# Kernel optimization log

Measured on AMD Instinct MI355X. Metric: run time of the kernel, lower is better.

Reference implementation:

```python
import jax, jax.numpy as jnp
import numpy as np

B, D, H, C = 8192, 384, 256, 6
K_MIN, K_MAX = 4, 16
LN_EPS = 1e-5


def setup_inputs() -> dict:
    key = jax.random.key(0)
    ks = jax.random.split(key, 6)
    s = lambda k, shape: (jax.random.normal(k, shape, jnp.float32) * 0.05)
    return {
        "x": jax.random.normal(ks[0], (B, D), jnp.float32),
        "W_proj": s(ks[1], (D, H)), "b_proj": jnp.zeros((H,), jnp.float32),
        "W_tau": s(ks[2], (D, 1)), "b_tau": jnp.zeros((1,), jnp.float32),
        "W_res": s(ks[3], (H, H)), "b_res": jnp.zeros((H,), jnp.float32),
        "ln_g": jnp.ones((H,), jnp.float32), "ln_b": jnp.zeros((H,), jnp.float32),
        "W_fc": s(ks[4], (H, C)), "b_fc": jnp.zeros((C,), jnp.float32),
    }


def reference(x, W_proj, b_proj, W_tau, b_tau, W_res, b_res, ln_g, ln_b, W_fc, b_fc):
    # adaptive k per sample (torch path casts to int -> non-differentiable)
    tau = jax.nn.sigmoid(x @ W_tau + b_tau)[:, 0]                      # [B]
    k = jax.lax.stop_gradient(
        jnp.clip(jnp.round(K_MAX - (K_MAX - K_MIN) * tau), 1, K_MAX)
    ).astype(jnp.int32)                                                # [B]

    # pairwise squared distances (same nearest-neighbor ordering as cdist)
    sq = jnp.sum(x * x, axis=-1)                                       # [B]
    d2 = sq[:, None] + sq[None, :] - 2.0 * (x @ x.T)                   # [B,B]
    _, idx = jax.lax.top_k(-jax.lax.stop_gradient(d2), K_MAX)          # [B,K_MAX] nearest (incl. self)

    h = jax.nn.relu(x @ W_proj + b_proj)                               # [B,H]

    # ragged top-k mean via fixed K_MAX gather + position mask
    gathered = h[idx]                                                  # [B,K_MAX,H]
    mask = (jnp.arange(K_MAX)[None, :] < k[:, None]).astype(h.dtype)   # [B,K_MAX]
    agg = jnp.einsum('bkh,bk->bh', gathered, mask) / k[:, None].astype(h.dtype)

    r = jax.nn.relu(agg @ W_res + b_res)                               # [B,H]
    z = h + r
    mu = jnp.mean(z, axis=-1, keepdims=True)
    var = jnp.var(z, axis=-1, keepdims=True)
    zn = (z - mu) / jnp.sqrt(var + LN_EPS)
    return (zn * ln_g + ln_b) @ W_fc + b_fc                            # [B,C]
```

## Files before the change

kernel.cpp:

```cpp
#include <hip/hip_runtime.h>
#include <hip/hip_fp16.h>
#include <math.h>

#define NROWS 8192
#define DDIM 384
#define HDIM 256
#define CDIM 6
#define LN_EPS 1e-5f
#define DSTR 138
#define NTILES ((NROWS/128) * (NROWS/128 + 1) / 2)
#define NGEMM1 ((NROWS/128) * (HDIM/128))

typedef short bf16x8 __attribute__((ext_vector_type(8)));
typedef float f32x4 __attribute__((ext_vector_type(4)));
typedef unsigned short u16x8 __attribute__((ext_vector_type(8)));
typedef unsigned short u16x4 __attribute__((ext_vector_type(4)));
typedef unsigned short u16x2 __attribute__((ext_vector_type(2)));

__device__ __forceinline__ bool dj_better(float d1, int j1, float d2, int j2) {
    return (d1 < d2) || (d1 == d2 && j1 < j2);
}

__device__ __forceinline__ unsigned int umin_(unsigned int a, unsigned int b) { return a < b ? a : b; }
__device__ __forceinline__ unsigned int umax_(unsigned int a, unsigned int b) { return a > b ? a : b; }

__device__ __forceinline__ unsigned short map16f(float v) {
    union { _Float16 f; unsigned short u; } c;
    c.f = (_Float16)v;
    unsigned short b = c.u;
    return (unsigned short)(b ^ (unsigned short)((((short)b) >> 15) | 0x8000));
}

__device__ __forceinline__ float unmap16(unsigned int m16b) {
    unsigned short fb = (m16b & 0x8000u) ? (unsigned short)(m16b ^ 0x8000u)
                                         : (unsigned short)(~m16b);
    union { unsigned short u; _Float16 f; } cv; cv.u = fb;
    return (float)cv.f;
}

__device__ __forceinline__ unsigned short rne_bf16(float v) {
    unsigned int u = __float_as_uint(v);
    u += 0x7fffu + ((u >> 16) & 1u);
    return (unsigned short)(u >> 16);
}

__device__ __forceinline__ void ins8(
    unsigned int& s0, unsigned int& s1, unsigned int& s2, unsigned int& s3,
    unsigned int& s4, unsigned int& s5, unsigned int& s6, unsigned int& s7,
    unsigned int& m, unsigned int key)
{
    if (key < m) {
        s0 = (s0 == m) ? key : s0;
        s1 = (s1 == m) ? key : s1;
        s2 = (s2 == m) ? key : s2;
        s3 = (s3 == m) ? key : s3;
        s4 = (s4 == m) ? key : s4;
        s5 = (s5 == m) ? key : s5;
        s6 = (s6 == m) ? key : s6;
        s7 = (s7 == m) ? key : s7;
        m = umax_(umax_(umax_(s0, s1), umax_(s2, s3)),
                  umax_(umax_(s4, s5), umax_(s6, s7)));
    }
}

__device__ __forceinline__ unsigned int max8_(
    unsigned int s0, unsigned int s1, unsigned int s2, unsigned int s3,
    unsigned int s4, unsigned int s5, unsigned int s6, unsigned int s7)
{
    return umax_(umax_(umax_(s0, s1), umax_(s2, s3)),
                 umax_(umax_(s4, s5), umax_(s6, s7)));
}

__device__ __forceinline__ void sins8(
    unsigned int& s0, unsigned int& s1, unsigned int& s2, unsigned int& s3,
    unsigned int& s4, unsigned int& s5, unsigned int& s6, unsigned int& s7,
    unsigned int key)
{
    unsigned int t = umin_(s0, key);
    s0 = umax_(t, s1); t = umin_(t, s1);
    s1 = umax_(t, s2); t = umin_(t, s2);
    s2 = umax_(t, s3); t = umin_(t, s3);
    s3 = umax_(t, s4); t = umin_(t, s4);
    s4 = umax_(t, s5); t = umin_(t, s5);
    s5 = umax_(t, s6); t = umin_(t, s6);
    s6 = umax_(t, s7); s7 = umin_(t, s7);
}

#define CE_(a, b) { unsigned int hi_ = umax_(a, b), lo_ = umin_(a, b); a = hi_; b = lo_; }
#define SORT8_DESC(s0, s1, s2, s3, s4, s5, s6, s7) \
    CE_(s0, s1) CE_(s2, s3) CE_(s4, s5) CE_(s6, s7) \
    CE_(s0, s2) CE_(s1, s3) CE_(s4, s6) CE_(s5, s7) \
    CE_(s1, s2) CE_(s5, s6) CE_(s0, s4) CE_(s3, s7) \
    CE_(s1, s5) CE_(s2, s6) \
    CE_(s1, s4) CE_(s3, s6) \
    CE_(s2, s4) CE_(s3, s5) \
    CE_(s3, s4)

__global__ void __launch_bounds__(256) prep_kernel(
    const float* __restrict__ x, const float* __restrict__ W_tau,
    const float* __restrict__ b_tau, unsigned short* __restrict__ xb,
    float* __restrict__ sq, int* __restrict__ kk,
    const float* __restrict__ Wp, unsigned short* __restrict__ wpT,
    const float* __restrict__ Wr, unsigned short* __restrict__ wrT)
{
    int tid = threadIdx.x;
    if (blockIdx.x < NROWS / 4) {
        int wave = tid >> 6, lane = tid & 63;
        int row = blockIdx.x * 4 + wave;
        const float* xr = x + (size_t)row * DDIM;
        unsigned short* xbr = xb + (size_t)row * DDIM;
        float s = 0.f, tp = 0.f;
        #pragma unroll
        for (int q = 0; q < 6; ++q) {
            float v = xr[lane + 64 * q];
            xbr[lane + 64 * q] = rne_bf16(v);
            s = fmaf(v, v, s);
            tp = fmaf(v, W_tau[lane + 64 * q], tp);
        }
        #pragma unroll
        for (int off = 32; off > 0; off >>= 1) {
            s += __shfl_xor(s, off);
            tp += __shfl_xor(tp, off);
        }
        if (lane == 0) {
            sq[row] = s;
            float u = tp + b_tau[0];
            float tau = 1.f / (1.f + expf(-u));
            float kf = rintf(16.f - 12.f * tau);
            int k = (int)kf;
            k = min(16, max(1, k));
            kk[row] = k;
        }
    } else {
        int i = (blockIdx.x - NROWS / 4) * 256 + tid;
        if (i < DDIM * HDIM) {
            int k = i / HDIM, n = i % HDIM;
            wpT[(size_t)n * DDIM + k] = rne_bf16(Wp[i]);
        } else {
            int j = i - DDIM * HDIM;
            if (j < HDIM * HDIM) {
                int k = j / HDIM, n = j % HDIM;
                wrT[(size_t)n * HDIM + k] = rne_bf16(Wr[j]);
            }
        }
    }
}

__device__ __forceinline__ void gemm_kloop(
    const unsigned short* __restrict__ A, const unsigned short* __restrict__ B,
    const int K, const int rowbase, const int nbase,
    unsigned short* S, f32x4 (&acc)[4][4])
{
    const int tid = threadIdx.x;
    const int wave = tid >> 6;
    const int lane = tid & 63;
    const int wr = (wave >> 1) * 64;
    const int wc = (wave & 1) * 64;
    const int m16 = lane & 15;
    const int kq = lane >> 4;
    const int er0 = tid >> 2;
    const int er1 = 64 + (tid >> 2);
    const int eko = tid & 3;
    const int NK = K >> 5;

    auto stage = [&](int kb, int set) {
        const int k0 = kb * 32;
        char* Ad = (char*)S + set * 8192;
        char* Bd = (char*)S + 16384 + set * 8192;
        __builtin_amdgcn_global_load_lds(
            (const __attribute__((address_space(1))) void*)(A + (size_t)(rowbase + er0) * K + k0 + eko * 8),
            (__attribute__((address_space(3))) void*)(Ad + (wave * 64) * 16), 16, 0, 0);
        __builtin_amdgcn_global_load_lds(
            (const __attribute__((address_space(1))) void*)(A + (size_t)(rowbase + er1) * K + k0 + eko * 8),
            (__attribute__((address_space(3))) void*)(Ad + (256 + wave * 64) * 16), 16, 0, 0);
        __builtin_amdgcn_global_load_lds(
            (const __attribute__((address_space(1))) void*)(B + (size_t)(nbase + er0) * K + k0 + eko * 8),
            (__attribute__((address_space(3))) void*)(Bd + (wave * 64) * 16), 16, 0, 0);
        __builtin_amdgcn_global_load_lds(
            (const __attribute__((address_space(1))) void*)(B + (size_t)(nbase + er1) * K + k0 + eko * 8),
            (__attribute__((address_space(3))) void*)(Bd + (256 + wave * 64) * 16), 16, 0, 0);
    };

    stage(0, 0);
    stage(1, 1);
    asm volatile("s_waitcnt vmcnt(4)" ::: "memory");
    __builtin_amdgcn_s_barrier();
    __builtin_amdgcn_sched_barrier(0);

    for (int kb = 0; kb < NK; ++kb) {
        const int cur = kb & 1;
        const unsigned short* Ab = S + cur * 4096;
        const unsigned short* Bb = S + 8192 + cur * 4096;
        bf16x8 af[4], bfr[4];
        #pragma unroll
        for (int s = 0; s < 4; ++s) {
            af[s]  = *(const bf16x8*)&Ab[(wr + s * 16 + m16) * 32 + kq * 8];
            bfr[s] = *(const bf16x8*)&Bb[(wc + s * 16 + m16) * 32 + kq * 8];
        }
        #pragma unroll
        for (int si = 0; si < 4; ++si)
            #pragma unroll
            for (int sj = 0; sj < 4; ++sj)
                acc[si][sj] = __builtin_amdgcn_mfma_f32_16x16x32_bf16(
                    af[si], bfr[sj], acc[si][sj], 0, 0, 0);
        asm volatile("s_waitcnt lgkmcnt(0)" ::: "memory");
        __builtin_amdgcn_s_barrier();
        __builtin_amdgcn_sched_barrier(0);
        if (kb + 2 < NK) {
            stage(kb + 2, cur);
            asm volatile("s_waitcnt vmcnt(4)" ::: "memory");
            __builtin_amdgcn_s_barrier();
            __builtin_amdgcn_sched_barrier(0);
        } else if (kb + 1 < NK) {
            asm volatile("s_waitcnt vmcnt(0)" ::: "memory");
            __builtin_amdgcn_s_barrier();
            __builtin_amdgcn_sched_barrier(0);
        }
    }
}

__device__ __forceinline__ void gemm_epilogue(
    const float* __restrict__ bias, float* __restrict__ out,
    unsigned short* __restrict__ hb, const int rowbase, const int nbase,
    f32x4 (&acc)[4][4])
{
    const int lane = threadIdx.x & 63;
    const int wave = threadIdx.x >> 6;
    const int wr = (wave >> 1) * 64;
    const int wc = (wave & 1) * 64;
    const int m16 = lane & 15;
    const int kq = lane >> 4;
    #pragma unroll
    for (int sj = 0; sj < 4; ++sj) {
        int c = nbase + wc + sj * 16 + m16;
        float bc = bias[c];
        #pragma unroll
        for (int si = 0; si < 4; ++si) {
            int r = rowbase + wr + si * 16 + kq * 4;
            #pragma unroll
            for (int v = 0; v < 4; ++v) {
                float val = fmaxf(acc[si][sj][v] + bc, 0.f);
                out[(size_t)(r + v) * HDIM + c] = val;
                if (hb) hb[(size_t)(r + v) * HDIM + c] = rne_bf16(val);
            }
        }
    }
}

__global__ void __launch_bounds__(256) mfma_gemm_bias_relu_kernel(
    const unsigned short* __restrict__ A, const unsigned short* __restrict__ WT,
    const float* __restrict__ bias, float* __restrict__ out,
    unsigned short* __restrict__ hb, int K)
{
    __shared__ __align__(16) unsigned short S[16384];
    f32x4 acc[4][4];
    #pragma unroll
    for (int a = 0; a < 4; ++a)
        #pragma unroll
        for (int b = 0; b < 4; ++b)
            acc[a][b] = (f32x4){0.f, 0.f, 0.f, 0.f};
    gemm_kloop(A, WT, K, blockIdx.x * 128, blockIdx.y * 128, S, acc);
    gemm_epilogue(bias, out, hb, blockIdx.x * 128, blockIdx.y * 128, acc);
}

__global__ void __launch_bounds__(256) dist_gemm_fused_kernel(
    const unsigned short* __restrict__ xb, const float* __restrict__ sq,
    unsigned int* __restrict__ keys,
    const unsigned short* __restrict__ wpT, const float* __restrict__ b_proj,
    float* __restrict__ h, unsigned short* __restrict__ hb)
{
    __shared__ __align__(16) unsigned short SMEM[128 * DSTR];

    f32x4 acc[4][4];
    #pragma unroll
    for (int a = 0; a < 4; ++a)
        #pragma unroll
        for (int b = 0; b < 4; ++b)
            acc[a][b] = (f32x4){0.f, 0.f, 0.f, 0.f};

    if (blockIdx.x < NGEMM1) {
        const int rb = (blockIdx.x >> 1) * 128;
        const int nb = (blockIdx.x & 1) * 128;
        gemm_kloop(xb, wpT, DDIM, rb, nb, SMEM, acc);
        gemm_epilogue(b_proj, h, hb, rb, nb, acc);
        return;
    }

    int t0 = blockIdx.x - NGEMM1;
    int t = (t0 & 7) * (NTILES / 8) + (t0 >> 3);
    int bi = (int)((sqrtf(8.f * (float)t + 1.f) - 1.f) * 0.5f);
    while ((bi + 1) * (bi + 2) / 2 <= t) ++bi;
    while (bi * (bi + 1) / 2 > t) --bi;
    int bj = t - bi * (bi + 1) / 2;

    const int tid = threadIdx.x;
    const int wave = tid >> 6;
    const int lane = tid & 63;
    const int rowbase = bi * 128;
    const int colbase = bj * 128;
    const int wr = (wave >> 1) * 64;
    const int wc = (wave & 1) * 64;
    const int m16 = lane & 15;
    const int kq = lane >> 4;

    gemm_kloop(xb, xb, DDIM, rowbase, colbase, SMEM, acc);
    __syncthreads();
    unsigned short* Dt = SMEM;

    const int sr = tid >> 1;
    const int seg = tid & 1;

    {
        float sqc[4];
        #pragma unroll
        for (int sj = 0; sj < 4; ++sj) sqc[sj] = sq[colbase + wc + sj * 16 + m16];
        #pragma unroll
        for (int si = 0; si < 4; ++si)
            #pragma unroll
            for (int sj = 0; sj < 4; ++sj) {
                int r = wr + si * 16 + kq * 4;
                int c = wc + sj * 16 + m16;
                #pragma unroll
                for (int v = 0; v < 4; ++v)
                    Dt[(r + v) * DSTR + c] = map16f(sqc[sj] - 2.0f * acc[si][sj][v]);
            }
        __syncthreads();

        const unsigned short* rowp = &Dt[sr * DSTR + seg * 64];
        const int cb0 = colbase + seg * 64;
        u16x8 c0 = *(const u16x8*)rowp;
        unsigned int s0 = ((unsigned int)c0[0] << 13) | (unsigned int)(cb0 + 0);
        unsigned int s1 = ((unsigned int)c0[1] << 13) | (unsigned int)(cb0 + 1);
        unsigned int s2 = ((unsigned int)c0[2] << 13) | (unsigned int)(cb0 + 2);
        unsigned int s3 = ((unsigned int)c0[3] << 13) | (unsigned int)(cb0 + 3);
        unsigned int s4 = ((unsigned int)c0[4] << 13) | (unsigned int)(cb0 + 4);
        unsigned int s5 = ((unsigned int)c0[5] << 13) | (unsigned int)(cb0 + 5);
        unsigned int s6 = ((unsigned int)c0[6] << 13) | (unsigned int)(cb0 + 6);
        unsigned int s7 = ((unsigned int)c0[7] << 13) | (unsigned int)(cb0 + 7);
        SORT8_DESC(s0, s1, s2, s3, s4, s5, s6, s7);
        #pragma unroll
        for (int i = 1; i < 8; ++i) {
            u16x8 ch = *(const u16x8*)(rowp + i * 8);
            int cb = cb0 + i * 8;
            #pragma unroll
            for (int e = 0; e < 8; ++e)
                sins8(s0, s1, s2, s3, s4, s5, s6, s7,
                      ((unsigned int)ch[e] << 13) | (unsigned int)(cb + e));
        }
        size_t kb = (size_t)(rowbase + sr) * 1024 + (size_t)bj * 16 + seg * 8;
        uint4 o0; o0.x = s0; o0.y = s1; o0.z = s2; o0.w = s3;
        uint4 o1; o1.x = s4; o1.y = s5; o1.z = s6; o1.w = s7;
        *(uint4*)&keys[kb] = o0;
        *(uint4*)&keys[kb + 4] = o1;
    }

    if (bi != bj) {
        __syncthreads();
        #pragma unroll
        for (int si = 0; si < 4; ++si) {
            float4 sqr4 = *(const float4*)&sq[rowbase + wr + si * 16 + kq * 4];
            float srw[4] = {sqr4.x, sqr4.y, sqr4.z, sqr4.w};
            #pragma unroll
            for (int sj = 0; sj < 4; ++sj) {
                int r = wr + si * 16 + kq * 4;
                int c = wc + sj * 16 + m16;
                unsigned short h4[4];
                #pragma unroll
                for (int v = 0; v < 4; ++v)
                    h4[v] = map16f(srw[v] - 2.0f * acc[si][sj][v]);
                *(unsigned long long*)&Dt[c * DSTR + r] = *(unsigned long long*)h4;
            }
        }
        __syncthreads();

        const unsigned short* rowp = &Dt[sr * DSTR + seg * 64];
        const int cb0 = rowbase + seg * 64;
        u16x8 c0 = *(const u16x8*)rowp;
        unsigned int s0 = ((unsigned int)c0[0] << 13) | (unsigned int)(cb0 + 0);
        unsigned int s1 = ((unsigned int)c0[1] << 13) | (unsigned int)(cb0 + 1);
        unsigned int s2 = ((unsigned int)c0[2] << 13) | (unsigned int)(cb0 + 2);
        unsigned int s3 = ((unsigned int)c0[3] << 13) | (unsigned int)(cb0 + 3);
        unsigned int s4 = ((unsigned int)c0[4] << 13) | (unsigned int)(cb0 + 4);
        unsigned int s5 = ((unsigned int)c0[5] << 13) | (unsigned int)(cb0 + 5);
        unsigned int s6 = ((unsigned int)c0[6] << 13) | (unsigned int)(cb0 + 6);
        unsigned int s7 = ((unsigned int)c0[7] << 13) | (unsigned int)(cb0 + 7);
        SORT8_DESC(s0, s1, s2, s3, s4, s5, s6, s7);
        #pragma unroll
        for (int i = 1; i < 8; ++i) {
            u16x8 ch = *(const u16x8*)(rowp + i * 8);
            int cb = cb0 + i * 8;
            #pragma unroll
            for (int e = 0; e < 8; ++e)
                sins8(s0, s1, s2, s3, s4, s5, s6, s7,
                      ((unsigned int)ch[e] << 13) | (unsigned int)(cb + e));
        }
        size_t kb = (size_t)(colbase + sr) * 1024 + (size_t)bi * 16 + seg * 8;
        uint4 o0; o0.x = s0; o0.y = s1; o0.z = s2; o0.w = s3;
        uint4 o1; o1.x = s4; o1.y = s5; o1.z = s6; o1.w = s7;
        *(uint4*)&keys[kb] = o0;
        *(uint4*)&keys[kb + 4] = o1;
    }
}

__global__ void __launch_bounds__(256) topk_rescore_agg_kernel(
    const unsigned int* __restrict__ keys, const float* __restrict__ x,
    const float* __restrict__ sq, const int* __restrict__ kk,
    const unsigned short* __restrict__ hb, unsigned short* __restrict__ aggb)
{
    const int w = threadIdx.x >> 6;
    const int row = blockIdx.x * 4 + w;
    const int lane = threadIdx.x & 63;
    __shared__ int sidx[4][16];

    const uint4* kp = (const uint4*)(keys + (size_t)row * 1024 + lane * 16);
    uint4 v0 = kp[0], v1 = kp[1];
    unsigned int s0 = v0.x, s1 = v0.y, s2 = v0.z, s3 = v0.w;
    unsigned int s4 = v1.x, s5 = v1.y, s6 = v1.z, s7 = v1.w;
    unsigned int m = max8_(s0, s1, s2, s3, s4, s5, s6, s7);
    #pragma unroll
    for (int q = 2; q < 4; ++q) {
        uint4 v = kp[q];
        unsigned int gmin = umin_(umin_(v.x, v.y), umin_(v.z, v.w));
        if (gmin < m) {
            ins8(s0, s1, s2, s3, s4, s5, s6, s7, m, v.x);
            ins8(s0, s1, s2, s3, s4, s5, s6, s7, m, v.y);
            ins8(s0, s1, s2, s3, s4, s5, s6, s7, m, v.z);
            ins8(s0, s1, s2, s3, s4, s5, s6, s7, m, v.w);
        }
    }
    unsigned int lmin = umin_(umin_(umin_(s0, s1), umin_(s2, s3)),
                              umin_(umin_(s4, s5), umin_(s6, s7)));
    unsigned int myout = 0;
    for (int t = 0; t < 32; ++t) {
        unsigned int wv = lmin;
        #pragma unroll
        for (int off = 32; off > 0; off >>= 1)
            wv = umin_(wv, (unsigned int)__shfl_xor((int)wv, off));
        if (lane == t) myout = wv;
        if (lmin == wv) {
            s0 = (s0 == wv) ? 0xFFFFFFFFu : s0;
            s1 = (s1 == wv) ? 0xFFFFFFFFu : s1;
            s2 = (s2 == wv) ? 0xFFFFFFFFu : s2;
            s3 = (s3 == wv) ? 0xFFFFFFFFu : s3;
            s4 = (s4 == wv) ? 0xFFFFFFFFu : s4;
            s5 = (s5 == wv) ? 0xFFFFFFFFu : s5;
            s6 = (s6 == wv) ? 0xFFFFFFFFu : s6;
            s7 = (s7 == wv) ? 0xFFFFFFFFu : s7;
            lmin = umin_(umin_(umin_(s0, s1), umin_(s2, s3)),
                         umin_(umin_(s4, s5), umin_(s6, s7)));
        }
    }
    int myj = (int)(myout & 8191u);
    float dscr = (lane < 32) ? unmap16(myout >> 13) : INFINITY;

    const float EPS2 = 2.5f;
    const int k = kk[row];
    float d_k   = __shfl(dscr, k);
    float d_km1 = __shfl(dscr, k - 1);
    bool cin = false, amb = false;
    if (lane < 32) {
        if (lane < k) { cin = (dscr + EPS2 <= d_k); amb = !cin; }
        else          { amb = (dscr < d_km1 + EPS2); }
    }
    unsigned long long cinmask = __ballot(cin);
    unsigned long long ambmask = __ballot(amb);
    int n_in = __popcll(cinmask);
    int msel = k - n_in;

    float d_ex = 0.f;
    if (msel > 0) {
        float xr[6];
        #pragma unroll
        for (int q = 0; q < 6; ++q) xr[q] = x[(size_t)row * DDIM + lane + 64 * q];
        float sqrow = sq[row];
        unsigned long long mm = ambmask;
        while (mm) {
            int c = (int)(__ffsll(mm) - 1);
            mm &= mm - 1;
            int j = __shfl(myj, c);
            const float* xc = x + (size_t)j * DDIM;
            float p = 0.f;
            #pragma unroll
            for (int q = 0; q < 6; ++q) p = fmaf(xr[q], xc[lane + 64 * q], p);
            #pragma unroll
            for (int off = 32; off > 0; off >>= 1) p += __shfl_xor(p, off);
            float d = sqrow + sq[j] - 2.f * p;
            if (lane == c) d_ex = d;
        }
        int selrank = 0;
        unsigned long long mm2 = ambmask;
        while (mm2) {
            int u = (int)(__ffsll(mm2) - 1);
            mm2 &= mm2 - 1;
            float du = __shfl(d_ex, u);
            int ju = __shfl(myj, u);
            if (u != lane && dj_better(du, ju, d_ex, myj)) ++selrank;
        }
        if (amb && selrank < msel)
            sidx[w][n_in + selrank] = myj;
    }
    if (cin) {
        int pos = __popcll(cinmask & ((1ull << lane) - 1ull));
        sidx[w][pos] = myj;
    }
    __syncthreads();

    float a0 = 0.f, a1 = 0.f, a2 = 0.f, a3 = 0.f;
    for (int t = 0; t < k; ++t) {
        uint2 v = *(const uint2*)(hb + (size_t)sidx[w][t] * HDIM + lane * 4);
        a0 += __uint_as_float(v.x << 16);
        a1 += __uint_as_float(v.x & 0xFFFF0000u);
        a2 += __uint_as_float(v.y << 16);
        a3 += __uint_as_float(v.y & 0xFFFF0000u);
    }
    float inv = 1.f / (float)k;
    unsigned int b0 = rne_bf16(a0 * inv);
    unsigned int b1 = rne_bf16(a1 * inv);
    unsigned int b2 = rne_bf16(a2 * inv);
    unsigned int b3 = rne_bf16(a3 * inv);
    uint2 o; o.x = b0 | (b1 << 16); o.y = b2 | (b3 << 16);
    *(uint2*)(aggb + (size_t)row * HDIM + lane * 4) = o;
}

__global__ void __launch_bounds__(256) ln_fc_kernel(
    const float* __restrict__ h, const float* __restrict__ r,
    const float* __restrict__ g, const float* __restrict__ bb,
    const float* __restrict__ W_fc, const float* __restrict__ b_fc,
    float* __restrict__ out)
{
    const int row = blockIdx.x * 4 + (threadIdx.x >> 6);
    const int lane = threadIdx.x & 63;
    const float* hp = h + (size_t)row * HDIM;
    const float* rp = r + (size_t)row * HDIM;

    float z[4];
    #pragma unroll
    for (int q = 0; q < 4; ++q)
        z[q] = hp[lane + 64 * q] + rp[lane + 64 * q];

    float s = z[0] + z[1] + z[2] + z[3];
    float s2 = z[0]*z[0] + z[1]*z[1] + z[2]*z[2] + z[3]*z[3];
    #pragma unroll
    for (int off = 32; off > 0; off >>= 1) {
        s += __shfl_xor(s, off);
        s2 += __shfl_xor(s2, off);
    }
    float mu = s / 256.f;
    float rstd = rsqrtf(s2 / 256.f - mu * mu + LN_EPS);

    float p[6] = {0.f, 0.f, 0.f, 0.f, 0.f, 0.f};
    #pragma unroll
    for (int q = 0; q < 4; ++q) {
        int i = lane + 64 * q;
        float val = (z[q] - mu) * rstd * g[i] + bb[i];
        #pragma unroll
        for (int c = 0; c < 6; ++c)
            p[c] = fmaf(val, W_fc[i * 6 + c], p[c]);
    }
    #pragma unroll
    for (int c = 0; c < 6; ++c)
        #pragma unroll
        for (int off = 32; off > 0; off >>= 1) p[c] += __shfl_xor(p[c], off);

    if (lane < 6) {
        float o = p[0];
        o = (lane == 1) ? p[1] : o;
        o = (lane == 2) ? p[2] : o;
        o = (lane == 3) ? p[3] : o;
        o = (lane == 4) ? p[4] : o;
        o = (lane == 5) ? p[5] : o;
        out[(size_t)row * CDIM + lane] = o + b_fc[lane];
    }
}

extern "C" void kernel_launch(void* const* d_in, const int* in_sizes, int n_in,
                              void* d_out, int out_size, void* d_ws, size_t ws_size,
                              hipStream_t stream) {
    const float* x      = (const float*)d_in[0];
    const float* W_proj = (const float*)d_in[1];
    const float* b_proj = (const float*)d_in[2];
    const float* W_tau  = (const float*)d_in[3];
    const float* b_tau  = (const float*)d_in[4];
    const float* W_res  = (const float*)d_in[5];
    const float* b_res  = (const float*)d_in[6];
    const float* ln_g   = (const float*)d_in[7];
    const float* ln_b   = (const float*)d_in[8];
    const float* W_fc   = (const float*)d_in[9];
    const float* b_fc   = (const float*)d_in[10];
    float* out = (float*)d_out;

    char* ws = (char*)d_ws;
    float* sq   = (float*)ws;                        ws += (size_t)NROWS * 4;
    int*   kk   = (int*)ws;                          ws += (size_t)NROWS * 4;
    float* h    = (float*)ws;                        ws += (size_t)NROWS * HDIM * 4;
    float* r    = (float*)ws;                        ws += (size_t)NROWS * HDIM * 4;
    unsigned short* xb   = (unsigned short*)ws;      ws += (size_t)NROWS * DDIM * 2;
    unsigned short* hbuf = (unsigned short*)ws;      ws += (size_t)NROWS * HDIM * 2;
    unsigned short* aggb = (unsigned short*)ws;      ws += (size_t)NROWS * HDIM * 2;
    unsigned short* wpT  = (unsigned short*)ws;      ws += (size_t)DDIM * HDIM * 2;
    unsigned short* wrT  = (unsigned short*)ws;      ws += (size_t)HDIM * HDIM * 2;
    ws = (char*)(((size_t)ws + 255) & ~(size_t)255);
    unsigned int* keys = (unsigned int*)ws;          ws += (size_t)NROWS * 1024 * 4;

    const int prepW = (DDIM * HDIM + HDIM * HDIM + 255) / 256;
    prep_kernel<<<NROWS / 4 + prepW, 256, 0, stream>>>(
        x, W_tau, b_tau, xb, sq, kk, W_proj, wpT, W_res, wrT);
    dist_gemm_fused_kernel<<<NGEMM1 + NTILES, 256, 0, stream>>>(
        xb, sq, keys, wpT, b_proj, h, hbuf);
    topk_rescore_agg_kernel<<<NROWS / 4, 256, 0, stream>>>(keys, x, sq, kk, hbuf, aggb);
    mfma_gemm_bias_relu_kernel<<<dim3(NROWS / 128, HDIM / 128), 256, 0, stream>>>(
        aggb, wrT, b_res, r, (unsigned short*)nullptr, HDIM);
    ln_fc_kernel<<<NROWS / 4, 256, 0, stream>>>(h, r, ln_g, ln_b, W_fc, b_fc, out);
}
```

Before: 223.6 us.

## Split top-k scan into dual chains and transpose per-tile key layout

```diff
diff --git a/kernel.cpp b/kernel.cpp
--- a/kernel.cpp
+++ b/kernel.cpp
@@ -10,12 +10,12 @@
 #define DSTR 138
 #define NTILES ((NROWS/128) * (NROWS/128 + 1) / 2)
 #define NGEMM1 ((NROWS/128) * (HDIM/128))
+#define KSTRIDE ((size_t)NROWS * 16)
 
 typedef short bf16x8 __attribute__((ext_vector_type(8)));
 typedef float f32x4 __attribute__((ext_vector_type(4)));
 typedef unsigned short u16x8 __attribute__((ext_vector_type(8)));
-typedef unsigned short u16x4 __attribute__((ext_vector_type(4)));
-typedef unsigned short u16x2 __attribute__((ext_vector_type(2)));
+typedef unsigned int u32x4 __attribute__((ext_vector_type(4)));
 
 __device__ __forceinline__ bool dj_better(float d1, int j1, float d2, int j2) {
     return (d1 < d2) || (d1 == d2 && j1 < j2);
@@ -71,30 +71,67 @@
                  umax_(umax_(s4, s5), umax_(s6, s7)));
 }
 
-__device__ __forceinline__ void sins8(
-    unsigned int& s0, unsigned int& s1, unsigned int& s2, unsigned int& s3,
-    unsigned int& s4, unsigned int& s5, unsigned int& s6, unsigned int& s7,
-    unsigned int key)
-{
-    unsigned int t = umin_(s0, key);
-    s0 = umax_(t, s1); t = umin_(t, s1);
-    s1 = umax_(t, s2); t = umin_(t, s2);
-    s2 = umax_(t, s3); t = umin_(t, s3);
-    s3 = umax_(t, s4); t = umin_(t, s4);
-    s4 = umax_(t, s5); t = umin_(t, s5);
-    s5 = umax_(t, s6); t = umin_(t, s6);
-    s6 = umax_(t, s7); s7 = umin_(t, s7);
+__device__ __forceinline__ void sins8a(unsigned int (&s)[8], unsigned int key)
+{
+    unsigned int t = umin_(s[0], key);
+    s[0] = umax_(t, s[1]); t = umin_(t, s[1]);
+    s[1] = umax_(t, s[2]); t = umin_(t, s[2]);
+    s[2] = umax_(t, s[3]); t = umin_(t, s[3]);
+    s[3] = umax_(t, s[4]); t = umin_(t, s[4]);
+    s[4] = umax_(t, s[5]); t = umin_(t, s[5]);
+    s[5] = umax_(t, s[6]); t = umin_(t, s[6]);
+    s[6] = umax_(t, s[7]); s[7] = umin_(t, s[7]);
 }
 
 #define CE_(a, b) { unsigned int hi_ = umax_(a, b), lo_ = umin_(a, b); a = hi_; b = lo_; }
-#define SORT8_DESC(s0, s1, s2, s3, s4, s5, s6, s7) \
-    CE_(s0, s1) CE_(s2, s3) CE_(s4, s5) CE_(s6, s7) \
-    CE_(s0, s2) CE_(s1, s3) CE_(s4, s6) CE_(s5, s7) \
-    CE_(s1, s2) CE_(s5, s6) CE_(s0, s4) CE_(s3, s7) \
-    CE_(s1, s5) CE_(s2, s6) \
-    CE_(s1, s4) CE_(s3, s6) \
-    CE_(s2, s4) CE_(s3, s5) \
-    CE_(s3, s4)
+#define SORT8A_DESC(s) \
+    CE_(s[0], s[1]) CE_(s[2], s[3]) CE_(s[4], s[5]) CE_(s[6], s[7]) \
+    CE_(s[0], s[2]) CE_(s[1], s[3]) CE_(s[4], s[6]) CE_(s[5], s[7]) \
+    CE_(s[1], s[2]) CE_(s[5], s[6]) CE_(s[0], s[4]) CE_(s[3], s[7]) \
+    CE_(s[1], s[5]) CE_(s[2], s[6]) \
+    CE_(s[1], s[4]) CE_(s[3], s[6]) \
+    CE_(s[2], s[4]) CE_(s[3], s[5]) \
+    CE_(s[3], s[4])
+
+__device__ __forceinline__ void scan_seed(
+    const unsigned short* rowp, int cb0, unsigned int (&s)[8])
+{
+    u16x8 c0 = *(const u16x8*)rowp;
+    s[0] = ((unsigned int)c0[0] << 13) | (unsigned int)(cb0 + 0);
+    s[1] = ((unsigned int)c0[1] << 13) | (unsigned int)(cb0 + 1);
+    s[2] = ((unsigned int)c0[2] << 13) | (unsigned int)(cb0 + 2);
+    s[3] = ((unsigned int)c0[3] << 13) | (unsigned int)(cb0 + 3);
+    s[4] = ((unsigned int)c0[4] << 13) | (unsigned int)(cb0 + 4);
+    s[5] = ((unsigned int)c0[5] << 13) | (unsigned int)(cb0 + 5);
+    s[6] = ((unsigned int)c0[6] << 13) | (unsigned int)(cb0 + 6);
+    s[7] = ((unsigned int)c0[7] << 13) | (unsigned int)(cb0 + 7);
+    SORT8A_DESC(s)
+}
+
+__device__ __forceinline__ void scan_chunk_i(
+    const unsigned short* rowp, int cb0, int i, unsigned int (&s)[8])
+{
+    u16x8 ch = *(const u16x8*)(rowp + i * 8);
+    int cb = cb0 + i * 8;
+    #pragma unroll
+    for (int e = 0; e < 8; ++e)
+        sins8a(s, ((unsigned int)ch[e] << 13) | (unsigned int)(cb + e));
+}
+
+__device__ __forceinline__ void scan_half_dual(
+    const unsigned short* rowp, int cb0, unsigned int (&SA)[8])
+{
+    unsigned int SB[8];
+    scan_seed(rowp, cb0, SA);
+    scan_seed(rowp + 8, cb0 + 8, SB);
+    #pragma unroll
+    for (int i = 2; i < 8; i += 2) {
+        scan_chunk_i(rowp, cb0, i, SA);
+        scan_chunk_i(rowp, cb0, i + 1, SB);
+    }
+    #pragma unroll
+    for (int e = 0; e < 8; ++e) sins8a(SA, SB[e]);
+}
 
 __global__ void __launch_bounds__(256) prep_kernel(
     const float* __restrict__ x, const float* __restrict__ W_tau,
@@ -309,6 +346,7 @@
 
     const int sr = tid >> 1;
     const int seg = tid & 1;
+    const unsigned short* rowp = &Dt[sr * DSTR + seg * 64];
 
     {
         float sqc[4];
@@ -326,32 +364,13 @@
             }
         __syncthreads();
 
-        const unsigned short* rowp = &Dt[sr * DSTR + seg * 64];
-        const int cb0 = colbase + seg * 64;
-        u16x8 c0 = *(const u16x8*)rowp;
-        unsigned int s0 = ((unsigned int)c0[0] << 13) | (unsigned int)(cb0 + 0);
-        unsigned int s1 = ((unsigned int)c0[1] << 13) | (unsigned int)(cb0 + 1);
-        unsigned int s2 = ((unsigned int)c0[2] << 13) | (unsigned int)(cb0 + 2);
-        unsigned int s3 = ((unsigned int)c0[3] << 13) | (unsigned int)(cb0 + 3);
-        unsigned int s4 = ((unsigned int)c0[4] << 13) | (unsigned int)(cb0 + 4);
-        unsigned int s5 = ((unsigned int)c0[5] << 13) | (unsigned int)(cb0 + 5);
-        unsigned int s6 = ((unsigned int)c0[6] << 13) | (unsigned int)(cb0 + 6);
-        unsigned int s7 = ((unsigned int)c0[7] << 13) | (unsigned int)(cb0 + 7);
-        SORT8_DESC(s0, s1, s2, s3, s4, s5, s6, s7);
-        #pragma unroll
-        for (int i = 1; i < 8; ++i) {
-            u16x8 ch = *(const u16x8*)(rowp + i * 8);
-            int cb = cb0 + i * 8;
-            #pragma unroll
-            for (int e = 0; e < 8; ++e)
-                sins8(s0, s1, s2, s3, s4, s5, s6, s7,
-                      ((unsigned int)ch[e] << 13) | (unsigned int)(cb + e));
-        }
-        size_t kb = (size_t)(rowbase + sr) * 1024 + (size_t)bj * 16 + seg * 8;
-        uint4 o0; o0.x = s0; o0.y = s1; o0.z = s2; o0.w = s3;
-        uint4 o1; o1.x = s4; o1.y = s5; o1.z = s6; o1.w = s7;
-        *(uint4*)&keys[kb] = o0;
-        *(uint4*)&keys[kb + 4] = o1;
+        unsigned int SA[8];
+        scan_half_dual(rowp, colbase + seg * 64, SA);
+        size_t kb = (size_t)bj * KSTRIDE + (size_t)(rowbase + sr) * 16 + seg * 8;
+        u32x4 o0 = {SA[0], SA[1], SA[2], SA[3]};
+        u32x4 o1 = {SA[4], SA[5], SA[6], SA[7]};
+        __builtin_nontemporal_store(o0, (u32x4*)&keys[kb]);
+        __builtin_nontemporal_store(o1, (u32x4*)&keys[kb + 4]);
     }
 
     if (bi != bj) {
@@ -373,32 +392,13 @@
         }
         __syncthreads();
 
-        const unsigned short* rowp = &Dt[sr * DSTR + seg * 64];
-        const int cb0 = rowbase + seg * 64;
-        u16x8 c0 = *(const u16x8*)rowp;
-        unsigned int s0 = ((unsigned int)c0[0] << 13) | (unsigned int)(cb0 + 0);
-        unsigned int s1 = ((unsigned int)c0[1] << 13) | (unsigned int)(cb0 + 1);
-        unsigned int s2 = ((unsigned int)c0[2] << 13) | (unsigned int)(cb0 + 2);
-        unsigned int s3 = ((unsigned int)c0[3] << 13) | (unsigned int)(cb0 + 3);
-        unsigned int s4 = ((unsigned int)c0[4] << 13) | (unsigned int)(cb0 + 4);
-        unsigned int s5 = ((unsigned int)c0[5] << 13) | (unsigned int)(cb0 + 5);
-        unsigned int s6 = ((unsigned int)c0[6] << 13) | (unsigned int)(cb0 + 6);
-        unsigned int s7 = ((unsigned int)c0[7] << 13) | (unsigned int)(cb0 + 7);
-        SORT8_DESC(s0, s1, s2, s3, s4, s5, s6, s7);
-        #pragma unroll
-        for (int i = 1; i < 8; ++i) {
-            u16x8 ch = *(const u16x8*)(rowp + i * 8);
-            int cb = cb0 + i * 8;
-            #pragma unroll
-            for (int e = 0; e < 8; ++e)
-                sins8(s0, s1, s2, s3, s4, s5, s6, s7,
-                      ((unsigned int)ch[e] << 13) | (unsigned int)(cb + e));
-        }
-        size_t kb = (size_t)(colbase + sr) * 1024 + (size_t)bi * 16 + seg * 8;
-        uint4 o0; o0.x = s0; o0.y = s1; o0.z = s2; o0.w = s3;
-        uint4 o1; o1.x = s4; o1.y = s5; o1.z = s6; o1.w = s7;
-        *(uint4*)&keys[kb] = o0;
-        *(uint4*)&keys[kb + 4] = o1;
+        unsigned int SA[8];
+        scan_half_dual(rowp, rowbase + seg * 64, SA);
+        size_t kb = (size_t)bi * KSTRIDE + (size_t)(colbase + sr) * 16 + seg * 8;
+        u32x4 o0 = {SA[0], SA[1], SA[2], SA[3]};
+        u32x4 o1 = {SA[4], SA[5], SA[6], SA[7]};
+        __builtin_nontemporal_store(o0, (u32x4*)&keys[kb]);
+        __builtin_nontemporal_store(o1, (u32x4*)&keys[kb + 4]);
     }
 }
 
@@ -412,20 +412,21 @@
     const int lane = threadIdx.x & 63;
     __shared__ int sidx[4][16];
 
-    const uint4* kp = (const uint4*)(keys + (size_t)row * 1024 + lane * 16);
-    uint4 v0 = kp[0], v1 = kp[1];
-    unsigned int s0 = v0.x, s1 = v0.y, s2 = v0.z, s3 = v0.w;
-    unsigned int s4 = v1.x, s5 = v1.y, s6 = v1.z, s7 = v1.w;
+    const unsigned int* kpb = keys + (size_t)lane * KSTRIDE + (size_t)row * 16;
+    u32x4 a0 = __builtin_nontemporal_load((const u32x4*)kpb);
+    u32x4 a1 = __builtin_nontemporal_load((const u32x4*)(kpb + 4));
+    unsigned int s0 = a0[0], s1 = a0[1], s2 = a0[2], s3 = a0[3];
+    unsigned int s4 = a1[0], s5 = a1[1], s6 = a1[2], s7 = a1[3];
     unsigned int m = max8_(s0, s1, s2, s3, s4, s5, s6, s7);
     #pragma unroll
     for (int q = 2; q < 4; ++q) {
-        uint4 v = kp[q];
-        unsigned int gmin = umin_(umin_(v.x, v.y), umin_(v.z, v.w));
+        u32x4 v = __builtin_nontemporal_load((const u32x4*)(kpb + q * 4));
+        unsigned int gmin = umin_(umin_(v[0], v[1]), umin_(v[2], v[3]));
         if (gmin < m) {
-            ins8(s0, s1, s2, s3, s4, s5, s6, s7, m, v.x);
-            ins8(s0, s1, s2, s3, s4, s5, s6, s7, m, v.y);
-            ins8(s0, s1, s2, s3, s4, s5, s6, s7, m, v.z);
-            ins8(s0, s1, s2, s3, s4, s5, s6, s7, m, v.w);
+            ins8(s0, s1, s2, s3, s4, s5, s6, s7, m, v[0]);
+            ins8(s0, s1, s2, s3, s4, s5, s6, s7, m, v[1]);
+            ins8(s0, s1, s2, s3, s4, s5, s6, s7, m, v[2]);
+            ins8(s0, s1, s2, s3, s4, s5, s6, s7, m, v[3]);
         }
     }
     unsigned int lmin = umin_(umin_(umin_(s0, s1), umin_(s2, s3)),
@@ -505,19 +506,19 @@
     }
     __syncthreads();
 
-    float a0 = 0.f, a1 = 0.f, a2 = 0.f, a3 = 0.f;
+    float a0f = 0.f, a1f = 0.f, a2f = 0.f, a3f = 0.f;
     for (int t = 0; t < k; ++t) {
         uint2 v = *(const uint2*)(hb + (size_t)sidx[w][t] * HDIM + lane * 4);
-        a0 += __uint_as_float(v.x << 16);
-        a1 += __uint_as_float(v.x & 0xFFFF0000u);
-        a2 += __uint_as_float(v.y << 16);
-        a3 += __uint_as_float(v.y & 0xFFFF0000u);
+        a0f += __uint_as_float(v.x << 16);
+        a1f += __uint_as_float(v.x & 0xFFFF0000u);
+        a2f += __uint_as_float(v.y << 16);
+        a3f += __uint_as_float(v.y & 0xFFFF0000u);
     }
     float inv = 1.f / (float)k;
-    unsigned int b0 = rne_bf16(a0 * inv);
-    unsigned int b1 = rne_bf16(a1 * inv);
-    unsigned int b2 = rne_bf16(a2 * inv);
-    unsigned int b3 = rne_bf16(a3 * inv);
+    unsigned int b0 = rne_bf16(a0f * inv);
+    unsigned int b1 = rne_bf16(a1f * inv);
+    unsigned int b2 = rne_bf16(a2f * inv);
+    unsigned int b3 = rne_bf16(a3f * inv);
     uint2 o; o.x = b0 | (b1 << 16); o.y = b2 | (b3 << 16);
     *(uint2*)(aggb + (size_t)row * HDIM + lane * 4) = o;
 }
```

Measured after the change: 231.9 us. 3.7% more time.
